# Optimization experiments

Measured on AMD Instinct MI355X. Metric: run time of the kernel, lower is better.

Reference implementation:

```python
import jax, jax.numpy as jnp
import numpy as np

B, S, H, D = 2, 4096, 16, 128
TILE = 128
T = S // TILE          # 32 tiles
TOPK = 7               # anchor-selected tiles per query tile (local tile appended -> 8)
DM = H * D
NEG = -1e10


def setup_inputs() -> dict:
    key = jax.random.key(0)
    ks = jax.random.split(key, 6)
    x = jax.random.normal(ks[0], (B, S, DM), dtype=jnp.float32)
    wq = jax.random.normal(ks[1], (DM, H * D), dtype=jnp.float32) * 0.02
    wk = jax.random.normal(ks[2], (DM, H * D), dtype=jnp.float32) * 0.02
    wv = jax.random.normal(ks[3], (DM, H * D), dtype=jnp.float32) * 0.02
    wo = jax.random.normal(ks[4], (H * D, DM), dtype=jnp.float32) * 0.02
    # RoPE tables (real/imag of freqs_cis), LLaMA-style
    inv_freq = 1.0 / (10000.0 ** (np.arange(0, D, 2, dtype=np.float32) / D))  # [D/2]
    t = np.arange(S, dtype=np.float32)
    freqs = np.outer(t, inv_freq)  # [S, D/2]
    cos = jnp.asarray(np.cos(freqs), dtype=jnp.float32)
    sin = jnp.asarray(np.sin(freqs), dtype=jnp.float32)
    anchor_indices = jax.random.randint(ks[5], (B, H, T, TOPK), 0, T, dtype=jnp.int32)
    return {"x": x, "wq": wq, "wk": wk, "wv": wv, "wo": wo,
            "cos": cos, "sin": sin, "anchor_indices": anchor_indices}


def _apply_rope(q, k, cos, sin):
    # q,k: [B,H,S,D]; cos,sin: [S,D/2]
    cos_f = jnp.concatenate([cos, cos], axis=-1)[None, None]  # [1,1,S,D]
    sin_f = jnp.concatenate([sin, sin], axis=-1)[None, None]

    def rot_half(x):
        h = x.shape[-1] // 2
        return jnp.concatenate([-x[..., h:], x[..., :h]], axis=-1)

    return q * cos_f + rot_half(q) * sin_f, k * cos_f + rot_half(k) * sin_f


def reference(x, wq, wk, wv, wo, cos, sin, anchor_indices):
    b, s, _ = x.shape
    h = anchor_indices.shape[1]
    t = anchor_indices.shape[2]
    tile = s // t
    d = wq.shape[1] // h

    q = (x @ wq).reshape(b, s, h, d).transpose(0, 2, 1, 3)  # [B,H,S,D]
    k = (x @ wk).reshape(b, s, h, d).transpose(0, 2, 1, 3)
    v = (x @ wv).reshape(b, s, h, d).transpose(0, 2, 1, 3)
    q, k = _apply_rope(q, k, cos, sin)

    # append local tile to anchor-selected tiles -> [B,H,T,K+1]
    local = jnp.broadcast_to(jnp.arange(t, dtype=jnp.int32)[None, None, :, None], (b, h, t, 1))
    tile_sel = jnp.concatenate([anchor_indices, local], axis=-1)
    # token indices of gathered tiles: [B,H,T,(K+1)*tile]
    offs = jnp.arange(tile, dtype=jnp.int32)[None, None, None, None, :]
    tok_idx = (tile_sel[..., None] * tile + offs)
    sparse_len = tile_sel.shape[-1] * tile
    flat_idx = jnp.clip(tok_idx.reshape(b, h, t, sparse_len), 0, s - 1)

    # gather K/V tiles: [B,H,T,L,D]
    gid = flat_idx.reshape(b, h, t * sparse_len)
    k_sp = jnp.take_along_axis(k, gid[..., None], axis=2).reshape(b, h, t, sparse_len, d)
    v_sp = jnp.take_along_axis(v, gid[..., None], axis=2).reshape(b, h, t, sparse_len, d)

    q_t = q.reshape(b, h, t, tile, d)
    logits = jnp.einsum('bhtqd,bhtkd->bhtqk', q_t, k_sp) / jnp.sqrt(jnp.float32(d))

    # causal future-mask within gathered set
    q_pos = jnp.arange(s, dtype=jnp.int32).reshape(t, tile)
    fut = flat_idx[:, :, :, None, :] > q_pos[None, None, :, :, None]  # [B,H,T,tile,L]
    logits = jnp.where(fut, NEG, logits)
    weights = jax.nn.softmax(logits, axis=-1)
    all_masked = jnp.all(fut, axis=-1, keepdims=True)
    weights = jnp.where(all_masked, 0.0, weights)
    weights = jnp.where(jnp.isnan(weights), 0.0, weights)

    out = jnp.einsum('bhtqk,bhtkd->bhtqd', weights, v_sp)
    out = out.reshape(b, h, s, d).transpose(0, 2, 1, 3).reshape(b, s, h * d)
    return out @ wo
```

## Files before the change

### kernel.cpp

```cpp
#include <hip/hip_runtime.h>
#include <hip/hip_bf16.h>


typedef __bf16 bf16_t;
using bf16x8 = __attribute__((ext_vector_type(8))) __bf16;
using bf16x4 = __attribute__((ext_vector_type(4))) __bf16;
using f32x4  = __attribute__((ext_vector_type(4))) float;

typedef const __attribute__((address_space(1))) void* gas_ptr;
typedef __attribute__((address_space(3))) void* las_ptr;

__device__ __forceinline__ void async_copy16(const void* g, void* l) {
  __builtin_amdgcn_global_load_lds((gas_ptr)g, (las_ptr)l, 16, 0, 0);
}

__device__ __forceinline__ f32x4 mfma16x16x32(bf16x8 a, bf16x8 b, f32x4 c) {
  return __builtin_amdgcn_mfma_f32_16x16x32_bf16(a, b, c, 0, 0, 0);
}

__global__ void cvt_f32_bf16(const float* __restrict__ X, bf16_t* __restrict__ Y) {
  int idx = blockIdx.x * 256 + threadIdx.x;
  float4 v = ((const float4*)X)[idx];
  bf16x4 r;
  r.x = (bf16_t)v.x; r.y = (bf16_t)v.y; r.z = (bf16_t)v.z; r.w = (bf16_t)v.w;
  ((bf16x4*)Y)[idx] = r;
}

__global__ void wtrans(const float* __restrict__ W, bf16_t* __restrict__ Wt) {
  __shared__ bf16_t t[64][66];
  const int r0 = blockIdx.x * 64, c0 = blockIdx.y * 64;
  const int tx = threadIdx.x & 63, ty = threadIdx.x >> 6;
  #pragma unroll
  for (int i = 0; i < 16; ++i) {
    int r = ty + 4 * i;
    t[r][tx] = (bf16_t)W[(size_t)(r0 + r) * 2048 + c0 + tx];
  }
  __syncthreads();
  #pragma unroll
  for (int i = 0; i < 16; ++i) {
    int n = ty + 4 * i;
    Wt[(size_t)(c0 + n) * 2048 + r0 + tx] = t[tx][n];
  }
}

__global__ __launch_bounds__(512, 2) void gemm256(
    const bf16_t* __restrict__ A, const bf16_t* __restrict__ Bt,
    float* __restrict__ Cf, bf16_t* __restrict__ Cq, int mode)
{
  __shared__ bf16_t Apan[4][8192];
  __shared__ bf16_t Bpan[4][8192];
  const int bid = blockIdx.x;
  const int swz = (bid & 7) * 32 + (bid >> 3);
  const int bm = (swz >> 3) * 256, bn = (swz & 7) * 256;
  const int tid = threadIdx.x;
  const int w = tid >> 6, l = tid & 63;
  const int wr = w >> 2, wc = w & 3;
  const int fr = l & 15, g4 = l >> 4;

  const int c0 = tid, c1 = tid + 512;
  const int r0 = c0 >> 2, s0c = ((c0 & 3) ^ ((r0 >> 1) & 3)) * 8;
  const int r1 = c1 >> 2, s1c = ((c1 & 3) ^ ((r1 >> 1) & 3)) * 8;
  const bf16_t* aS0 = A  + (size_t)(bm + r0) * 2048 + s0c;
  const bf16_t* aS1 = A  + (size_t)(bm + r1) * 2048 + s1c;
  const bf16_t* bS0 = Bt + (size_t)(bn + r0) * 2048 + s0c;
  const bf16_t* bS1 = Bt + (size_t)(bn + r1) * 2048 + s1c;
  const int d0 = c0 * 16, d1 = c1 * 16;

  int aOff[8], bOff[4];
  #pragma unroll
  for (int m = 0; m < 8; ++m) {
    int R = wr * 128 + m * 16 + fr;
    aOff[m] = R * 64 + ((g4 ^ ((R >> 1) & 3)) << 4);
  }
  #pragma unroll
  for (int n = 0; n < 4; ++n) {
    int R = wc * 64 + n * 16 + fr;
    bOff[n] = R * 64 + ((g4 ^ ((R >> 1) & 3)) << 4);
  }

  f32x4 acc[8][4];
  #pragma unroll
  for (int m = 0; m < 8; ++m)
    #pragma unroll
    for (int n = 0; n < 4; ++n) acc[m][n] = (f32x4){0.f, 0.f, 0.f, 0.f};

  auto STAGE = [&](int phi2) {
    const int slot = phi2 & 3;
    const int kb = phi2 * 32;
    char* dA = (char*)&Apan[slot][0];
    char* dB = (char*)&Bpan[slot][0];
    async_copy16(aS0 + kb, dA + d0);
    async_copy16(aS1 + kb, dA + d1);
    async_copy16(bS0 + kb, dB + d0);
    async_copy16(bS1 + kb, dB + d1);
  };

  STAGE(0);
  STAGE(1);
  __syncthreads();

  #pragma unroll 1
  for (int phi = 0; phi < 64; ++phi) {
    const int slot = phi & 3;
    const char* pa = (const char*)&Apan[slot][0];
    const char* pb = (const char*)&Bpan[slot][0];
    bf16x8 af[8], bfr[4];
    #pragma unroll
    for (int m = 0; m < 8; ++m) af[m] = *(const bf16x8*)(pa + aOff[m]);
    #pragma unroll
    for (int n = 0; n < 4; ++n) bfr[n] = *(const bf16x8*)(pb + bOff[n]);
    if (phi < 62) {
      STAGE(phi + 2);
      asm volatile("s_waitcnt vmcnt(4)" ::: "memory");
    } else {
      asm volatile("s_waitcnt vmcnt(0)" ::: "memory");
    }
    __builtin_amdgcn_sched_barrier(0);
    __builtin_amdgcn_s_barrier();
    __builtin_amdgcn_sched_barrier(0);
    __builtin_amdgcn_s_setprio(1);
    #pragma unroll
    for (int m = 0; m < 8; ++m)
      #pragma unroll
      for (int n = 0; n < 4; ++n)
        acc[m][n] = mfma16x16x32(af[m], bfr[n], acc[m][n]);
    __builtin_amdgcn_s_setprio(0);
    __builtin_amdgcn_sched_barrier(0);
  }

  if (mode == 2) {
    #pragma unroll
    for (int m = 0; m < 8; ++m)
      #pragma unroll
      for (int n = 0; n < 4; ++n) {
        int colv = bn + wc * 64 + n * 16 + fr;
        int h_ = colv >> 7, d_ = colv & 127;
        int row0 = bm + wr * 128 + m * 16 + g4 * 4;
        int b_ = row0 >> 12, sr = row0 & 4095;
        bf16x4 pk;
        #pragma unroll
        for (int j = 0; j < 4; ++j) pk[j] = (bf16_t)acc[m][n][j];
        *(bf16x4*)&Cq[(((size_t)(b_ * 16 + h_)) * 128 + d_) * 4096 + sr] = pk;
      }
    return;
  }

  #pragma unroll
  for (int m = 0; m < 8; ++m)
    #pragma unroll
    for (int n = 0; n < 4; ++n)
      #pragma unroll
      for (int j = 0; j < 4; ++j) {
        int row = bm + wr * 128 + m * 16 + g4 * 4 + j;
        int col = bn + wc * 64 + n * 16 + fr;
        if (mode == 0) {
          Cf[(size_t)row * 2048 + col] = acc[m][n][j];
        } else {
          int b = row >> 12, s = row & 4095, h = col >> 7, d = col & 127;
          Cq[(((size_t)(b * 16 + h)) * 4096 + s) * 128 + d] = (bf16_t)acc[m][n][j];
        }
      }
}

__global__ void rope_kernel(bf16_t* __restrict__ Q, bf16_t* __restrict__ K,
                            const float* __restrict__ cosT, const float* __restrict__ sinT)
{
  int gid = blockIdx.x * 4 + (threadIdx.x >> 6);
  int i = threadIdx.x & 63;
  bf16_t* p = ((gid < 131072) ? Q : K) + (size_t)(gid & 131071) * 128;
  int s = gid & 4095;
  float c = cosT[s * 64 + i], sn = sinT[s * 64 + i];
  float x0 = (float)p[i], x1 = (float)p[i + 64];
  p[i]      = (bf16_t)(x0 * c - x1 * sn);
  p[i + 64] = (bf16_t)(x1 * c + x0 * sn);
}

__global__ __launch_bounds__(256, 2) void attn_kernel(
    const bf16_t* __restrict__ Qf, const bf16_t* __restrict__ Kf,
    const bf16_t* __restrict__ Vt, const int* __restrict__ anchors,
    bf16_t* __restrict__ outB)
{
  __shared__ bf16_t Kl[2][8192];
  __shared__ bf16_t Vl[2][8192];
  __shared__ bf16_t Pbuf[4][2048];
  const int orig = blockIdx.x;
  const int blk = (orig & 7) * 128 + (orig >> 3);
  const int qt = 31 - (blk & 31);
  const int h = (blk >> 5) & 15, b = blk >> 9;
  const int bh = b * 16 + h;
  const int tid = threadIdx.x, w = tid >> 6, l = tid & 63;
  const int fr = l & 15, g4 = l >> 4;
  const float scale = 0.08838834764831845f;

  const int* anc = anchors + ((size_t)bh * 32 + qt) * 7;
  unsigned long long pk = 0;
  int nt = 0;
  #pragma unroll
  for (int t = 0; t < 7; ++t) {
    int v = anc[t];
    if (v <= qt) { pk |= (unsigned long long)v << (5 * nt); ++nt; }
  }
  pk |= (unsigned long long)qt << (5 * nt); ++nt;
  const int NS = nt * 2;

  const bf16_t* Qbase = Qf + (size_t)bh * 4096 * 128;
  const bf16_t* Kbase = Kf + (size_t)bh * 4096 * 128;
  const bf16_t* Vbase = Vt + (size_t)bh * 128 * 4096;
  char* P = (char*)&Pbuf[w][0];

  auto STAGE = [&](int tb2, int p) {
    const bf16_t* ksrc = Kbase + (size_t)tb2 * 128;
    const bf16_t* vsrc = Vbase + tb2;
    char* kd = (char*)&Kl[p][0];
    char* vd = (char*)&Vl[p][0];
    #pragma unroll
    for (int i = 0; i < 4; ++i) {
      int c = tid + i * 256;
      int kr = c >> 4, kcol = c & 15;
      async_copy16(ksrc + (size_t)kr * 128 + (size_t)((kcol ^ (kr & 7)) * 8),
                   kd + c * 16);
      int vr = c >> 3, vcol = c & 7;
      async_copy16(vsrc + (size_t)vr * 4096 + (size_t)((vcol ^ (vr & 7)) * 8),
                   vd + c * 16);
    }
  };

  bf16x8 aq[2][4];
  #pragma unroll
  for (int m = 0; m < 2; ++m) {
    int q = qt * 128 + w * 32 + m * 16 + fr;
    #pragma unroll
    for (int kc = 0; kc < 4; ++kc)
      aq[m][kc] = *(const bf16x8*)(Qbase + (size_t)q * 128 + kc * 32 + g4 * 8);
  }

  STAGE((int)(pk & 31) * 128, 0);
  __syncthreads();

  float mrun[2] = {-1e30f, -1e30f};
  float lrun[2] = {0.f, 0.f};
  f32x4 o[2][8];
  #pragma unroll
  for (int m = 0; m < 2; ++m)
    #pragma unroll
    for (int nd = 0; nd < 8; ++nd) o[m][nd] = (f32x4){0.f, 0.f, 0.f, 0.f};

  for (int s = 0; s < NS; ++s) {
    const int p = s & 1;
    const int ts = (int)((pk >> (5 * (s >> 1))) & 31);
    const bool domask = (ts == qt);
    if (s + 1 < NS) {
      int s1 = s + 1;
      int ts1 = (int)((pk >> (5 * (s1 >> 1))) & 31);
      STAGE(ts1 * 128 + (s1 & 1) * 64, p ^ 1);
    }

    f32x4 sc[4][2];
    #pragma unroll
    for (int n = 0; n < 4; ++n)
      #pragma unroll
      for (int m = 0; m < 2; ++m) sc[n][m] = (f32x4){0.f, 0.f, 0.f, 0.f};
    #pragma unroll
    for (int kc = 0; kc < 4; ++kc) {
      bf16x8 kf[4];
      #pragma unroll
      for (int n = 0; n < 4; ++n) {
        int r = n * 16 + fr;
        kf[n] = *(const bf16x8*)((const char*)&Kl[p][0] +
                 r * 256 + (((kc * 4 + g4) ^ (r & 7)) << 4));
      }
      #pragma unroll
      for (int n = 0; n < 4; ++n)
        #pragma unroll
        for (int m = 0; m < 2; ++m)
          sc[n][m] = mfma16x16x32(kf[n], aq[m][kc], sc[n][m]);
    }

    #pragma unroll
    for (int m = 0; m < 2; ++m) {
      const int q = m * 16 + fr;
      float rmax = -1e30f;
      if (domask) {
        const int qrow = w * 32 + m * 16 + fr;
        #pragma unroll
        for (int n = 0; n < 4; ++n)
          #pragma unroll
          for (int j = 0; j < 4; ++j) {
            float lg = sc[n][m][j] * scale;
            int tok = (s & 1) * 64 + n * 16 + g4 * 4 + j;
            if (tok > qrow) lg = -1e10f;
            sc[n][m][j] = lg;
            rmax = fmaxf(rmax, lg);
          }
      } else {
        #pragma unroll
        for (int n = 0; n < 4; ++n)
          #pragma unroll
          for (int j = 0; j < 4; ++j) {
            float lg = sc[n][m][j] * scale;
            sc[n][m][j] = lg;
            rmax = fmaxf(rmax, lg);
          }
      }
      rmax = fmaxf(rmax, __shfl_xor(rmax, 16));
      rmax = fmaxf(rmax, __shfl_xor(rmax, 32));
      if (__any(rmax > mrun[m] + 8.f)) {
        float mnew = fmaxf(mrun[m], rmax);
        float alpha = __expf(mrun[m] - mnew);
        lrun[m] *= alpha;
        #pragma unroll
        for (int nd = 0; nd < 8; ++nd)
          #pragma unroll
          for (int j = 0; j < 4; ++j) o[m][nd][j] *= alpha;
        mrun[m] = mnew;
      }
      float rsum = 0.f;
      #pragma unroll
      for (int n = 0; n < 4; ++n) {
        bf16x4 pkv;
        #pragma unroll
        for (int j = 0; j < 4; ++j) {
          float pe = __expf(sc[n][m][j] - mrun[m]);
          rsum += pe;
          pkv[j] = (bf16_t)pe;
        }
        int off = q * 128 + ((((n << 1) | (g4 >> 1)) ^ (q & 7)) << 4) + ((g4 & 1) << 3);
        *(bf16x4*)(P + off) = pkv;
      }
      rsum += __shfl_xor(rsum, 16);
      rsum += __shfl_xor(rsum, 32);
      lrun[m] += rsum;
    }

    #pragma unroll
    for (int kc2 = 0; kc2 < 2; ++kc2) {
      bf16x8 av[8];
      #pragma unroll
      for (int nd = 0; nd < 8; ++nd) {
        int r = nd * 16 + fr;
        av[nd] = *(const bf16x8*)((const char*)&Vl[p][0] +
                  r * 128 + (((kc2 * 4 + g4) ^ (r & 7)) << 4));
      }
      bf16x8 bp[2];
      #pragma unroll
      for (int m = 0; m < 2; ++m) {
        int q = m * 16 + fr;
        bp[m] = *(const bf16x8*)(P + q * 128 + ((((kc2 << 2) | g4) ^ (q & 7)) << 4));
      }
      #pragma unroll
      for (int nd = 0; nd < 8; ++nd)
        #pragma unroll
        for (int m = 0; m < 2; ++m)
          o[m][nd] = mfma16x16x32(av[nd], bp[m], o[m][nd]);
    }
    __syncthreads();
  }

  #pragma unroll
  for (int m = 0; m < 2; ++m) {
    float inv = 1.0f / lrun[m];
    #pragma unroll
    for (int nd = 0; nd < 8; ++nd) {
      bf16x4 pkv;
      #pragma unroll
      for (int j = 0; j < 4; ++j) pkv[j] = (bf16_t)(o[m][nd][j] * inv);
      int off = fr * 256 + ((((nd << 1) | (g4 >> 1)) ^ (fr & 7)) << 4) + ((g4 & 1) << 3);
      *(bf16x4*)(P + off) = pkv;
    }
    #pragma unroll
    for (int i = 0; i < 4; ++i) {
      int r = i * 4 + g4;
      int off = r * 256 + ((fr ^ (r & 7)) << 4);
      bf16x8 vrow = *(const bf16x8*)(P + off);
      size_t gaddr = (((size_t)b * 4096 + qt * 128 + w * 32 + m * 16 + r) * 2048)
                     + h * 128 + fr * 8;
      *(bf16x8*)(outB + gaddr) = vrow;
    }
  }
}

#define OFF_XB   ((size_t)0)
#define OFF_WQT  ((size_t)33554432)
#define OFF_WKT  ((size_t)41943040)
#define OFF_WVT  ((size_t)50331648)
#define OFF_WOT  ((size_t)58720256)
#define OFF_QF   ((size_t)67108864)
#define OFF_KF   ((size_t)100663296)
#define OFF_AT   ((size_t)134217728)
#define OFF_VT   ((size_t)167772160)

extern "C" void kernel_launch(void* const* d_in, const int* in_sizes, int n_in,
                              void* d_out, int out_size, void* d_ws, size_t ws_size,
                              hipStream_t stream) {
  (void)in_sizes; (void)n_in; (void)out_size; (void)ws_size;
  const float* x    = (const float*)d_in[0];
  const float* wq   = (const float*)d_in[1];
  const float* wk   = (const float*)d_in[2];
  const float* wv   = (const float*)d_in[3];
  const float* wo   = (const float*)d_in[4];
  const float* cosT = (const float*)d_in[5];
  const float* sinT = (const float*)d_in[6];
  const int*   anc  = (const int*)d_in[7];
  float* out = (float*)d_out;
  char* ws = (char*)d_ws;

  bf16_t* xb   = (bf16_t*)(ws + OFF_XB);
  bf16_t* wqt  = (bf16_t*)(ws + OFF_WQT);
  bf16_t* wkt  = (bf16_t*)(ws + OFF_WKT);
  bf16_t* wvt  = (bf16_t*)(ws + OFF_WVT);
  bf16_t* wot  = (bf16_t*)(ws + OFF_WOT);
  bf16_t* Qf   = (bf16_t*)(ws + OFF_QF);
  bf16_t* Kf   = (bf16_t*)(ws + OFF_KF);
  bf16_t* Vt   = (bf16_t*)(ws + OFF_VT);
  bf16_t* attnB = (bf16_t*)(ws + OFF_AT);

  cvt_f32_bf16<<<16384, 256, 0, stream>>>(x, xb);
  wtrans<<<dim3(32, 32), 256, 0, stream>>>(wq, wqt);
  wtrans<<<dim3(32, 32), 256, 0, stream>>>(wk, wkt);
  wtrans<<<dim3(32, 32), 256, 0, stream>>>(wv, wvt);
  wtrans<<<dim3(32, 32), 256, 0, stream>>>(wo, wot);
  gemm256<<<256, 512, 0, stream>>>(xb, wqt, nullptr, Qf, 1);
  gemm256<<<256, 512, 0, stream>>>(xb, wkt, nullptr, Kf, 1);
  gemm256<<<256, 512, 0, stream>>>(xb, wvt, nullptr, Vt, 2);
  rope_kernel<<<65536, 256, 0, stream>>>(Qf, Kf, cosT, sinT);
  attn_kernel<<<1024, 256, 0, stream>>>(Qf, Kf, Vt, anc, attnB);
  gemm256<<<256, 512, 0, stream>>>(attnB, wot, out, nullptr, 0);
}
```

Before: 401.0 us.

## Fuse QKV projections into one GEMM with RoPE epilogue, widen attention blocks

Concatenates the transposed Q/K/V weights so a single 768-block GEMM computes all three projections. RoPE is applied in the GEMM epilogue, which needs a wave tile of 64 rows by 128 columns so each wave holds a whole head's d and d+64 pairs, and the standalone rope kernel is dropped. The attention kernel moves to 512 threads with 16 query rows per wave, and the output staging buffer is reused from K LDS. This removes a kernel launch and the Q/K read-modify-write pass, but the RoPE epilogue does scalar bf16 stores and per-element cos/sin loads, and the new warp layout changes register pressure and occupancy.

Result: faster. 382.4 us (-4.6%).

```diff
diff --git a/kernel.cpp b/kernel.cpp
--- a/kernel.cpp
+++ b/kernel.cpp
@@ -45,16 +45,20 @@
 
 __global__ __launch_bounds__(512, 2) void gemm256(
     const bf16_t* __restrict__ A, const bf16_t* __restrict__ Bt,
-    float* __restrict__ Cf, bf16_t* __restrict__ Cq, int mode)
+    int nb, int mode, float* __restrict__ Cf,
+    bf16_t* __restrict__ outQ, bf16_t* __restrict__ outK,
+    bf16_t* __restrict__ outVT,
+    const float* __restrict__ cosT, const float* __restrict__ sinT)
 {
   __shared__ bf16_t Apan[4][8192];
   __shared__ bf16_t Bpan[4][8192];
   const int bid = blockIdx.x;
-  const int swz = (bid & 7) * 32 + (bid >> 3);
-  const int bm = (swz >> 3) * 256, bn = (swz & 7) * 256;
+  const int cpx = gridDim.x >> 3;
+  const int swz = (bid & 7) * cpx + (bid >> 3);
+  const int bm = (swz / nb) * 256, bn = (swz % nb) * 256;
   const int tid = threadIdx.x;
   const int w = tid >> 6, l = tid & 63;
-  const int wr = w >> 2, wc = w & 3;
+  const int wr = w >> 1, wc = w & 1;
   const int fr = l & 15, g4 = l >> 4;
 
   const int c0 = tid, c1 = tid + 512;
@@ -66,23 +70,23 @@
   const bf16_t* bS1 = Bt + (size_t)(bn + r1) * 2048 + s1c;
   const int d0 = c0 * 16, d1 = c1 * 16;
 
-  int aOff[8], bOff[4];
-  #pragma unroll
-  for (int m = 0; m < 8; ++m) {
-    int R = wr * 128 + m * 16 + fr;
+  int aOff[4], bOff[8];
+  #pragma unroll
+  for (int m = 0; m < 4; ++m) {
+    int R = wr * 64 + m * 16 + fr;
     aOff[m] = R * 64 + ((g4 ^ ((R >> 1) & 3)) << 4);
   }
   #pragma unroll
-  for (int n = 0; n < 4; ++n) {
-    int R = wc * 64 + n * 16 + fr;
+  for (int n = 0; n < 8; ++n) {
+    int R = wc * 128 + n * 16 + fr;
     bOff[n] = R * 64 + ((g4 ^ ((R >> 1) & 3)) << 4);
   }
 
-  f32x4 acc[8][4];
-  #pragma unroll
-  for (int m = 0; m < 8; ++m)
-    #pragma unroll
-    for (int n = 0; n < 4; ++n) acc[m][n] = (f32x4){0.f, 0.f, 0.f, 0.f};
+  f32x4 acc[4][8];
+  #pragma unroll
+  for (int m = 0; m < 4; ++m)
+    #pragma unroll
+    for (int n = 0; n < 8; ++n) acc[m][n] = (f32x4){0.f, 0.f, 0.f, 0.f};
 
   auto STAGE = [&](int phi2) {
     const int slot = phi2 & 3;
@@ -104,11 +108,11 @@
     const int slot = phi & 3;
     const char* pa = (const char*)&Apan[slot][0];
     const char* pb = (const char*)&Bpan[slot][0];
-    bf16x8 af[8], bfr[4];
-    #pragma unroll
-    for (int m = 0; m < 8; ++m) af[m] = *(const bf16x8*)(pa + aOff[m]);
-    #pragma unroll
-    for (int n = 0; n < 4; ++n) bfr[n] = *(const bf16x8*)(pb + bOff[n]);
+    bf16x8 af[4], bfr[8];
+    #pragma unroll
+    for (int m = 0; m < 4; ++m) af[m] = *(const bf16x8*)(pa + aOff[m]);
+    #pragma unroll
+    for (int n = 0; n < 8; ++n) bfr[n] = *(const bf16x8*)(pb + bOff[n]);
     if (phi < 62) {
       STAGE(phi + 2);
       asm volatile("s_waitcnt vmcnt(4)" ::: "memory");
@@ -120,69 +124,77 @@
     __builtin_amdgcn_sched_barrier(0);
     __builtin_amdgcn_s_setprio(1);
     #pragma unroll
-    for (int m = 0; m < 8; ++m)
-      #pragma unroll
-      for (int n = 0; n < 4; ++n)
+    for (int m = 0; m < 4; ++m)
+      #pragma unroll
+      for (int n = 0; n < 8; ++n)
         acc[m][n] = mfma16x16x32(af[m], bfr[n], acc[m][n]);
     __builtin_amdgcn_s_setprio(0);
     __builtin_amdgcn_sched_barrier(0);
   }
 
-  if (mode == 2) {
-    #pragma unroll
-    for (int m = 0; m < 8; ++m)
+  if (mode == 0) {
+    #pragma unroll
+    for (int m = 0; m < 4; ++m)
+      #pragma unroll
+      for (int n = 0; n < 8; ++n)
+        #pragma unroll
+        for (int j = 0; j < 4; ++j) {
+          int row = bm + wr * 64 + m * 16 + g4 * 4 + j;
+          int col = bn + wc * 128 + n * 16 + fr;
+          Cf[(size_t)row * 2048 + col] = acc[m][n][j];
+        }
+    return;
+  }
+
+  const int colbase = bn + wc * 128;
+  const int proj = colbase >> 11;
+  const int hh = (colbase & 2047) >> 7;
+  if (proj == 2) {
+    #pragma unroll
+    for (int m = 0; m < 4; ++m) {
+      int row0 = bm + wr * 64 + m * 16 + g4 * 4;
+      int b_ = row0 >> 12, sr = row0 & 4095;
+      #pragma unroll
+      for (int n = 0; n < 8; ++n) {
+        int d_ = n * 16 + fr;
+        bf16x4 pkv;
+        #pragma unroll
+        for (int j = 0; j < 4; ++j) pkv[j] = (bf16_t)acc[m][n][j];
+        *(bf16x4*)&outVT[(((size_t)(b_ * 16 + hh)) * 128 + d_) * 4096 + sr] = pkv;
+      }
+    }
+  } else {
+    bf16_t* dst = proj ? outK : outQ;
+    #pragma unroll
+    for (int m = 0; m < 4; ++m) {
+      int row0 = bm + wr * 64 + m * 16 + g4 * 4;
+      int b_ = row0 >> 12, s0 = row0 & 4095;
+      size_t hbase = ((size_t)(b_ * 16 + hh)) * 4096;
       #pragma unroll
       for (int n = 0; n < 4; ++n) {
-        int colv = bn + wc * 64 + n * 16 + fr;
-        int h_ = colv >> 7, d_ = colv & 127;
-        int row0 = bm + wr * 128 + m * 16 + g4 * 4;
-        int b_ = row0 >> 12, sr = row0 & 4095;
-        bf16x4 pk;
-        #pragma unroll
-        for (int j = 0; j < 4; ++j) pk[j] = (bf16_t)acc[m][n][j];
-        *(bf16x4*)&Cq[(((size_t)(b_ * 16 + h_)) * 128 + d_) * 4096 + sr] = pk;
-      }
-    return;
-  }
-
-  #pragma unroll
-  for (int m = 0; m < 8; ++m)
-    #pragma unroll
-    for (int n = 0; n < 4; ++n)
-      #pragma unroll
-      for (int j = 0; j < 4; ++j) {
-        int row = bm + wr * 128 + m * 16 + g4 * 4 + j;
-        int col = bn + wc * 64 + n * 16 + fr;
-        if (mode == 0) {
-          Cf[(size_t)row * 2048 + col] = acc[m][n][j];
-        } else {
-          int b = row >> 12, s = row & 4095, h = col >> 7, d = col & 127;
-          Cq[(((size_t)(b * 16 + h)) * 4096 + s) * 128 + d] = (bf16_t)acc[m][n][j];
+        int d = n * 16 + fr;
+        #pragma unroll
+        for (int j = 0; j < 4; ++j) {
+          int s = s0 + j;
+          float c  = cosT[s * 64 + d];
+          float sn = sinT[s * 64 + d];
+          float x0 = acc[m][n][j], x1 = acc[m][n + 4][j];
+          dst[(hbase + s) * 128 + d]      = (bf16_t)(x0 * c - x1 * sn);
+          dst[(hbase + s) * 128 + d + 64] = (bf16_t)(x1 * c + x0 * sn);
         }
       }
-}
-
-__global__ void rope_kernel(bf16_t* __restrict__ Q, bf16_t* __restrict__ K,
-                            const float* __restrict__ cosT, const float* __restrict__ sinT)
-{
-  int gid = blockIdx.x * 4 + (threadIdx.x >> 6);
-  int i = threadIdx.x & 63;
-  bf16_t* p = ((gid < 131072) ? Q : K) + (size_t)(gid & 131071) * 128;
-  int s = gid & 4095;
-  float c = cosT[s * 64 + i], sn = sinT[s * 64 + i];
-  float x0 = (float)p[i], x1 = (float)p[i + 64];
-  p[i]      = (bf16_t)(x0 * c - x1 * sn);
-  p[i + 64] = (bf16_t)(x1 * c + x0 * sn);
-}
-
-__global__ __launch_bounds__(256, 2) void attn_kernel(
+    }
+  }
+}
+
+__global__ __launch_bounds__(512, 4) void attn_kernel(
     const bf16_t* __restrict__ Qf, const bf16_t* __restrict__ Kf,
     const bf16_t* __restrict__ Vt, const int* __restrict__ anchors,
     bf16_t* __restrict__ outB)
 {
   __shared__ bf16_t Kl[2][8192];
   __shared__ bf16_t Vl[2][8192];
-  __shared__ bf16_t Pbuf[4][2048];
+  __shared__ bf16_t Pbuf[8][1024];
   const int orig = blockIdx.x;
   const int blk = (orig & 7) * 128 + (orig >> 3);
   const int qt = 31 - (blk & 31);
@@ -214,8 +226,8 @@
     char* kd = (char*)&Kl[p][0];
     char* vd = (char*)&Vl[p][0];
     #pragma unroll
-    for (int i = 0; i < 4; ++i) {
-      int c = tid + i * 256;
+    for (int i = 0; i < 2; ++i) {
+      int c = tid + i * 512;
       int kr = c >> 4, kcol = c & 15;
       async_copy16(ksrc + (size_t)kr * 128 + (size_t)((kcol ^ (kr & 7)) * 8),
                    kd + c * 16);
@@ -225,25 +237,19 @@
     }
   };
 
-  bf16x8 aq[2][4];
-  #pragma unroll
-  for (int m = 0; m < 2; ++m) {
-    int q = qt * 128 + w * 32 + m * 16 + fr;
-    #pragma unroll
-    for (int kc = 0; kc < 4; ++kc)
-      aq[m][kc] = *(const bf16x8*)(Qbase + (size_t)q * 128 + kc * 32 + g4 * 8);
-  }
+  const int qrow = qt * 128 + w * 16 + fr;
+  bf16x8 aq[4];
+  #pragma unroll
+  for (int kc = 0; kc < 4; ++kc)
+    aq[kc] = *(const bf16x8*)(Qbase + (size_t)qrow * 128 + kc * 32 + g4 * 8);
 
   STAGE((int)(pk & 31) * 128, 0);
   __syncthreads();
 
-  float mrun[2] = {-1e30f, -1e30f};
-  float lrun[2] = {0.f, 0.f};
-  f32x4 o[2][8];
-  #pragma unroll
-  for (int m = 0; m < 2; ++m)
-    #pragma unroll
-    for (int nd = 0; nd < 8; ++nd) o[m][nd] = (f32x4){0.f, 0.f, 0.f, 0.f};
+  float mrun = -1e30f, lrun = 0.f;
+  f32x4 o[8];
+  #pragma unroll
+  for (int nd = 0; nd < 8; ++nd) o[nd] = (f32x4){0.f, 0.f, 0.f, 0.f};
 
   for (int s = 0; s < NS; ++s) {
     const int p = s & 1;
@@ -255,11 +261,9 @@
       STAGE(ts1 * 128 + (s1 & 1) * 64, p ^ 1);
     }
 
-    f32x4 sc[4][2];
-    #pragma unroll
-    for (int n = 0; n < 4; ++n)
-      #pragma unroll
-      for (int m = 0; m < 2; ++m) sc[n][m] = (f32x4){0.f, 0.f, 0.f, 0.f};
+    f32x4 sc[4];
+    #pragma unroll
+    for (int n = 0; n < 4; ++n) sc[n] = (f32x4){0.f, 0.f, 0.f, 0.f};
     #pragma unroll
     for (int kc = 0; kc < 4; ++kc) {
       bf16x8 kf[4];
@@ -271,66 +275,60 @@
       }
       #pragma unroll
       for (int n = 0; n < 4; ++n)
-        #pragma unroll
-        for (int m = 0; m < 2; ++m)
-          sc[n][m] = mfma16x16x32(kf[n], aq[m][kc], sc[n][m]);
-    }
-
-    #pragma unroll
-    for (int m = 0; m < 2; ++m) {
-      const int q = m * 16 + fr;
-      float rmax = -1e30f;
-      if (domask) {
-        const int qrow = w * 32 + m * 16 + fr;
-        #pragma unroll
-        for (int n = 0; n < 4; ++n)
-          #pragma unroll
-          for (int j = 0; j < 4; ++j) {
-            float lg = sc[n][m][j] * scale;
-            int tok = (s & 1) * 64 + n * 16 + g4 * 4 + j;
-            if (tok > qrow) lg = -1e10f;
-            sc[n][m][j] = lg;
-            rmax = fmaxf(rmax, lg);
-          }
-      } else {
-        #pragma unroll
-        for (int n = 0; n < 4; ++n)
-          #pragma unroll
-          for (int j = 0; j < 4; ++j) {
-            float lg = sc[n][m][j] * scale;
-            sc[n][m][j] = lg;
-            rmax = fmaxf(rmax, lg);
-          }
+        sc[n] = mfma16x16x32(kf[n], aq[kc], sc[n]);
+    }
+
+    float rmax = -1e30f;
+    if (domask) {
+      const int qr = w * 16 + fr;
+      #pragma unroll
+      for (int n = 0; n < 4; ++n)
+        #pragma unroll
+        for (int j = 0; j < 4; ++j) {
+          float lg = sc[n][j] * scale;
+          int tok = (s & 1) * 64 + n * 16 + g4 * 4 + j;
+          if (tok > qr) lg = -1e10f;
+          sc[n][j] = lg;
+          rmax = fmaxf(rmax, lg);
+        }
+    } else {
+      #pragma unroll
+      for (int n = 0; n < 4; ++n)
+        #pragma unroll
+        for (int j = 0; j < 4; ++j) {
+          float lg = sc[n][j] * scale;
+          sc[n][j] = lg;
+          rmax = fmaxf(rmax, lg);
+        }
+    }
+    rmax = fmaxf(rmax, __shfl_xor(rmax, 16));
+    rmax = fmaxf(rmax, __shfl_xor(rmax, 32));
+    if (__any(rmax > mrun + 8.f)) {
+      float mnew = fmaxf(mrun, rmax);
+      float alpha = __expf(mrun - mnew);
+      lrun *= alpha;
+      #pragma unroll
+      for (int nd = 0; nd < 8; ++nd)
+        #pragma unroll
+        for (int j = 0; j < 4; ++j) o[nd][j] *= alpha;
+      mrun = mnew;
+    }
+    float rsum = 0.f;
+    #pragma unroll
+    for (int n = 0; n < 4; ++n) {
+      bf16x4 pkv;
+      #pragma unroll
+      for (int j = 0; j < 4; ++j) {
+        float pe = __expf(sc[n][j] - mrun);
+        rsum += pe;
+        pkv[j] = (bf16_t)pe;
       }
-      rmax = fmaxf(rmax, __shfl_xor(rmax, 16));
-      rmax = fmaxf(rmax, __shfl_xor(rmax, 32));
-      if (__any(rmax > mrun[m] + 8.f)) {
-        float mnew = fmaxf(mrun[m], rmax);
-        float alpha = __expf(mrun[m] - mnew);
-        lrun[m] *= alpha;
-        #pragma unroll
-        for (int nd = 0; nd < 8; ++nd)
-          #pragma unroll
-          for (int j = 0; j < 4; ++j) o[m][nd][j] *= alpha;
-        mrun[m] = mnew;
-      }
-      float rsum = 0.f;
-      #pragma unroll
-      for (int n = 0; n < 4; ++n) {
-        bf16x4 pkv;
-        #pragma unroll
-        for (int j = 0; j < 4; ++j) {
-          float pe = __expf(sc[n][m][j] - mrun[m]);
-          rsum += pe;
-          pkv[j] = (bf16_t)pe;
-        }
-        int off = q * 128 + ((((n << 1) | (g4 >> 1)) ^ (q & 7)) << 4) + ((g4 & 1) << 3);
-        *(bf16x4*)(P + off) = pkv;
-      }
-      rsum += __shfl_xor(rsum, 16);
-      rsum += __shfl_xor(rsum, 32);
-      lrun[m] += rsum;
-    }
+      int off = fr * 128 + ((((n << 1) | (g4 >> 1)) ^ (fr & 7)) << 4) + ((g4 & 1) << 3);
+      *(bf16x4*)(P + off) = pkv;
+    }
+    rsum += __shfl_xor(rsum, 16);
+    rsum += __shfl_xor(rsum, 32);
+    lrun += rsum;
 
     #pragma unroll
     for (int kc2 = 0; kc2 < 2; ++kc2) {
@@ -341,38 +339,31 @@
         av[nd] = *(const bf16x8*)((const char*)&Vl[p][0] +
                   r * 128 + (((kc2 * 4 + g4) ^ (r & 7)) << 4));
       }
-      bf16x8 bp[2];
-      #pragma unroll
-      for (int m = 0; m < 2; ++m) {
-        int q = m * 16 + fr;
-        bp[m] = *(const bf16x8*)(P + q * 128 + ((((kc2 << 2) | g4) ^ (q & 7)) << 4));
-      }
+      bf16x8 bp = *(const bf16x8*)(P + fr * 128 + ((((kc2 << 2) | g4) ^ (fr & 7)) << 4));
       #pragma unroll
       for (int nd = 0; nd < 8; ++nd)
-        #pragma unroll
-        for (int m = 0; m < 2; ++m)
-          o[m][nd] = mfma16x16x32(av[nd], bp[m], o[m][nd]);
+        o[nd] = mfma16x16x32(av[nd], bp, o[nd]);
     }
     __syncthreads();
   }
 
-  #pragma unroll
-  for (int m = 0; m < 2; ++m) {
-    float inv = 1.0f / lrun[m];
+  {
+    char* E = (char*)&Kl[0][0] + w * 4096;
+    float inv = 1.0f / lrun;
     #pragma unroll
     for (int nd = 0; nd < 8; ++nd) {
       bf16x4 pkv;
       #pragma unroll
-      for (int j = 0; j < 4; ++j) pkv[j] = (bf16_t)(o[m][nd][j] * inv);
+      for (int j = 0; j < 4; ++j) pkv[j] = (bf16_t)(o[nd][j] * inv);
       int off = fr * 256 + ((((nd << 1) | (g4 >> 1)) ^ (fr & 7)) << 4) + ((g4 & 1) << 3);
-      *(bf16x4*)(P + off) = pkv;
+      *(bf16x4*)(E + off) = pkv;
     }
     #pragma unroll
     for (int i = 0; i < 4; ++i) {
       int r = i * 4 + g4;
       int off = r * 256 + ((fr ^ (r & 7)) << 4);
-      bf16x8 vrow = *(const bf16x8*)(P + off);
-      size_t gaddr = (((size_t)b * 4096 + qt * 128 + w * 32 + m * 16 + r) * 2048)
+      bf16x8 vrow = *(const bf16x8*)(E + off);
+      size_t gaddr = (((size_t)b * 4096 + qt * 128 + w * 16 + r) * 2048)
                      + h * 128 + fr * 8;
       *(bf16x8*)(outB + gaddr) = vrow;
     }
@@ -380,9 +371,7 @@
 }
 
 #define OFF_XB   ((size_t)0)
-#define OFF_WQT  ((size_t)33554432)
-#define OFF_WKT  ((size_t)41943040)
-#define OFF_WVT  ((size_t)50331648)
+#define OFF_WCAT ((size_t)33554432)
 #define OFF_WOT  ((size_t)58720256)
 #define OFF_QF   ((size_t)67108864)
 #define OFF_KF   ((size_t)100663296)
@@ -405,9 +394,10 @@
   char* ws = (char*)d_ws;
 
   bf16_t* xb   = (bf16_t*)(ws + OFF_XB);
-  bf16_t* wqt  = (bf16_t*)(ws + OFF_WQT);
-  bf16_t* wkt  = (bf16_t*)(ws + OFF_WKT);
-  bf16_t* wvt  = (bf16_t*)(ws + OFF_WVT);
+  bf16_t* wcat = (bf16_t*)(ws + OFF_WCAT);
+  bf16_t* wqt  = wcat;
+  bf16_t* wkt  = wcat + (size_t)2048 * 2048;
+  bf16_t* wvt  = wcat + (size_t)4096 * 2048;
   bf16_t* wot  = (bf16_t*)(ws + OFF_WOT);
   bf16_t* Qf   = (bf16_t*)(ws + OFF_QF);
   bf16_t* Kf   = (bf16_t*)(ws + OFF_KF);
@@ -419,10 +409,8 @@
   wtrans<<<dim3(32, 32), 256, 0, stream>>>(wk, wkt);
   wtrans<<<dim3(32, 32), 256, 0, stream>>>(wv, wvt);
   wtrans<<<dim3(32, 32), 256, 0, stream>>>(wo, wot);
-  gemm256<<<256, 512, 0, stream>>>(xb, wqt, nullptr, Qf, 1);
-  gemm256<<<256, 512, 0, stream>>>(xb, wkt, nullptr, Kf, 1);
-  gemm256<<<256, 512, 0, stream>>>(xb, wvt, nullptr, Vt, 2);
-  rope_kernel<<<65536, 256, 0, stream>>>(Qf, Kf, cosT, sinT);
-  attn_kernel<<<1024, 256, 0, stream>>>(Qf, Kf, Vt, anc, attnB);
-  gemm256<<<256, 512, 0, stream>>>(attnB, wot, out, nullptr, 0);
-}
+  gemm256<<<768, 512, 0, stream>>>(xb, wcat, 24, 1, nullptr, Qf, Kf, Vt, cosT, sinT);
+  attn_kernel<<<1024, 512, 0, stream>>>(Qf, Kf, Vt, anc, attnB);
+  gemm256<<<256, 512, 0, stream>>>(attnB, wot, 8, 0, out, nullptr, nullptr, nullptr,
+                                   nullptr, nullptr);
+}
```
